# Optimization experiments

Measured on AMD Instinct MI355X. Metric: run time of the kernel, lower is better.

## Reference

```python
import jax, jax.numpy as jnp
import numpy as np

CONTEXT_LENGTH = 2048
D_MODEL = 1024
N_HEADS = 16
D_HEAD = 64
ROPE_BASE = 10000.0
STD = 0.02


def rope(x, sines, cosines):
    # x: [b, s, h, d]; sines/cosines: [s, d//2]; interleaved even/odd pairing
    x_even = x[..., ::2]
    x_odd = x[..., 1::2]
    c = cosines[None, :, None, :]
    s = sines[None, :, None, :]
    out_even = x_even * c - x_odd * s
    out_odd = x_even * s + x_odd * c
    return jnp.stack((out_even, out_odd), axis=-1).reshape(x.shape)


def setup_inputs() -> dict:
    key = jax.random.key(0)
    k1, k2, k3, k4, k5 = jax.random.split(key, 5)
    x = jax.random.normal(k1, (2, 2048, D_MODEL), dtype=jnp.float32)
    key_weight = STD * jax.random.normal(k2, (N_HEADS, D_HEAD, D_MODEL), dtype=jnp.float32)
    query_weight = STD * jax.random.normal(k3, (N_HEADS, D_HEAD, D_MODEL), dtype=jnp.float32)
    value_weight = STD * jax.random.normal(k4, (N_HEADS, D_HEAD, D_MODEL), dtype=jnp.float32)
    output_weight = STD * jax.random.normal(k5, (D_MODEL, N_HEADS, D_HEAD), dtype=jnp.float32)
    angles = ROPE_BASE ** (-2.0 * jnp.arange(D_HEAD // 2, dtype=jnp.float32) / D_HEAD)
    positions = jnp.arange(CONTEXT_LENGTH, dtype=jnp.float32)
    apos = positions[:, None] * angles[None, :]  # [context, d_head//2]
    sines = jnp.sin(apos)
    cosines = jnp.cos(apos)
    return {"x": x, "key_weight": key_weight, "query_weight": query_weight,
            "value_weight": value_weight, "output_weight": output_weight,
            "sines": sines, "cosines": cosines}


def reference(x, key_weight, query_weight, value_weight, output_weight, sines, cosines):
    s = x.shape[1]
    sn, cs = sines[:s], cosines[:s]
    keys = jnp.einsum('hdm,bpm->bphd', key_weight, x)
    queries = jnp.einsum('hdm,bpm->bphd', query_weight, x)
    values = jnp.einsum('hdm,bpm->bphd', value_weight, x)
    keys = rope(keys, sn, cs)
    queries = rope(queries, sn, cs)
    # NOTE: no 1/sqrt(d_head) scaling, faithful to source
    scores = jnp.einsum('bkhd,bqhd->bhqk', keys, queries)
    mask = jnp.tril(jnp.ones((s, s), dtype=bool))  # causal (task='next_token')
    scores = jnp.where(mask[None, None], scores, -jnp.inf)
    pattern = jax.nn.softmax(scores, axis=-1)
    outputs = jnp.einsum('bhqk,bkhd->bqhd', pattern, values)
    return jnp.einsum('mhd,bphd->bpm', output_weight, outputs)
```

## Files before the change

kernel.cpp:

```cpp
#include <hip/hip_runtime.h>
#include <hip/hip_bf16.h>
#include <stdint.h>

typedef __bf16 bf16_t;
typedef bf16_t bf16x8 __attribute__((ext_vector_type(8)));
typedef float  f32x4  __attribute__((ext_vector_type(4)));

#define GAS __attribute__((address_space(1)))
#define LAS __attribute__((address_space(3)))

__device__ inline void gld_lds16(const void* g, void* l) {
    __builtin_amdgcn_global_load_lds((const GAS void*)g, (LAS void*)l, 16, 0, 0);
}

__device__ inline int swz(int row, int colbyte) {
    return row * 128 + (colbyte ^ ((row & 7) << 4));
}

__global__ __launch_bounds__(256) void k_cvt5(const float* __restrict__ i0, bf16_t* __restrict__ o0,
                                              const float* __restrict__ i1, bf16_t* __restrict__ o1,
                                              const float* __restrict__ i2, bf16_t* __restrict__ o2,
                                              const float* __restrict__ i3, bf16_t* __restrict__ o3,
                                              const float* __restrict__ i4, bf16_t* __restrict__ o4) {
    const float* in; bf16_t* out; int n;
    switch (blockIdx.y) {
        case 0: in = i0; out = o0; n = 4194304; break;
        case 1: in = i1; out = o1; n = 1048576; break;
        case 2: in = i2; out = o2; n = 1048576; break;
        case 3: in = i3; out = o3; n = 1048576; break;
        default: in = i4; out = o4; n = 1048576; break;
    }
    int i = (blockIdx.x * 256 + threadIdx.x) * 8;
    if (i >= n) return;
    f32x4 v0 = *(const f32x4*)(in + i);
    f32x4 v1 = *(const f32x4*)(in + i + 4);
    bf16x8 o;
    o[0] = (bf16_t)v0[0]; o[1] = (bf16_t)v0[1]; o[2] = (bf16_t)v0[2]; o[3] = (bf16_t)v0[3];
    o[4] = (bf16_t)v1[0]; o[5] = (bf16_t)v1[1]; o[6] = (bf16_t)v1[2]; o[7] = (bf16_t)v1[3];
    *(bf16x8*)(out + i) = o;
}

__global__ __launch_bounds__(256) void k_rope(bf16_t* __restrict__ Q, bf16_t* __restrict__ Kt,
                                              const float* __restrict__ sn,
                                              const float* __restrict__ cs) {
    int idx = blockIdx.x * 256 + threadIdx.x;
    bf16_t* T = blockIdx.y ? Kt : Q;
    int row = idx >> 9;
    int pi  = idx & 511;
    int h = pi >> 5, i = pi & 31;
    int p = row & 2047;
    float c = cs[p * 32 + i], s = sn[p * 32 + i];
    bf16_t* ptr = T + (size_t)row * 1024 + h * 64 + 2 * i;
    float e = (float)ptr[0], o = (float)ptr[1];
    ptr[0] = (bf16_t)(e * c - o * s);
    ptr[1] = (bf16_t)(e * s + o * c);
}

template <typename OutT>
__global__ __launch_bounds__(256) void k_gemm_bt(
    const bf16_t* __restrict__ A,
    const bf16_t* __restrict__ B0, const bf16_t* __restrict__ B1,
    OutT* __restrict__ C0, OutT* __restrict__ C1,
    int M, int N, int K) {
    const bf16_t* B = blockIdx.z == 0 ? B0 : B1;
    OutT*         C = blockIdx.z == 0 ? C0 : C1;
    const int BK = 32;
    __shared__ bf16_t As[128 * BK];
    __shared__ bf16_t Bs[128 * BK];
    int tid = threadIdx.x;
    int lane = tid & 63, wid = tid >> 6;
    int row0 = blockIdx.y * 128, col0 = blockIdx.x * 128;
    int wr = (wid >> 1) * 64, wc = (wid & 1) * 64;
    int lr = lane & 15, kg = lane >> 4;

    f32x4 acc[4][4];
#pragma unroll
    for (int i = 0; i < 4; ++i)
#pragma unroll
        for (int j = 0; j < 4; ++j) acc[i][j] = (f32x4){0.f, 0.f, 0.f, 0.f};

    int ob = tid * 16;
    for (int k0 = 0; k0 < K; k0 += BK) {
        __syncthreads();
#pragma unroll
        for (int p = 0; p < 2; ++p) {
            int off = p * 4096 + ob;
            int r = off >> 6;
            int cb = off & 63;
            gld_lds16((const char*)A + ((size_t)(row0 + r) * K + k0) * 2 + cb, (char*)As + off);
            gld_lds16((const char*)B + ((size_t)(col0 + r) * K + k0) * 2 + cb, (char*)Bs + off);
        }
        __syncthreads();
        bf16x8 af[4], bfr[4];
#pragma unroll
        for (int mi = 0; mi < 4; ++mi)
            af[mi] = *(const bf16x8*)&As[(wr + mi * 16 + lr) * BK + kg * 8];
#pragma unroll
        for (int ni = 0; ni < 4; ++ni)
            bfr[ni] = *(const bf16x8*)&Bs[(wc + ni * 16 + lr) * BK + kg * 8];
#pragma unroll
        for (int mi = 0; mi < 4; ++mi)
#pragma unroll
            for (int ni = 0; ni < 4; ++ni)
                acc[mi][ni] = __builtin_amdgcn_mfma_f32_16x16x32_bf16(af[mi], bfr[ni],
                                                                      acc[mi][ni], 0, 0, 0);
    }
#pragma unroll
    for (int mi = 0; mi < 4; ++mi)
#pragma unroll
        for (int ni = 0; ni < 4; ++ni)
#pragma unroll
            for (int r = 0; r < 4; ++r) {
                int row = row0 + wr + mi * 16 + kg * 4 + r;
                int col = col0 + wc + ni * 16 + lr;
                C[(size_t)row * N + col] = (OutT)acc[mi][ni][r];
            }
}

__global__ __launch_bounds__(256) void k_flash(const bf16_t* __restrict__ Q,
                                               const bf16_t* __restrict__ Kt,
                                               const bf16_t* __restrict__ Vt,
                                               bf16_t* __restrict__ Ob) {
    const int DM = 1024, S = 2048;
    int qb = (blockIdx.y & 8) ? (31 - blockIdx.x) : blockIdx.x;
    int h = blockIdx.y, b = blockIdx.z;
    int tid = threadIdx.x, lane = tid & 63, wid = tid >> 6;
    int lr = lane & 15, kg = lane >> 4;
    int rowbase = b * S;
    int colbase = h * 64;

    __shared__ bf16_t Ks[2][64 * 64];
    __shared__ bf16_t Vs[2][64 * 64];
    __shared__ bf16_t Ps[4][16 * 64];

    int qrow0 = qb * 64 + wid * 16;
    bf16x8 qf[2];
#pragma unroll
    for (int s = 0; s < 2; ++s)
        qf[s] = *(const bf16x8*)&Q[(size_t)(rowbase + qrow0 + lr) * DM + colbase + s * 32 + kg * 8];

    f32x4 Oa[4];
    float m_run[4], l_run[4];
#pragma unroll
    for (int i = 0; i < 4; ++i) {
        Oa[i] = (f32x4){0.f, 0.f, 0.f, 0.f};
        m_run[i] = -1e30f;
        l_run[i] = 0.f;
    }

    int r0 = tid >> 3;
    int c0 = (tid & 7) * 8;
    const bf16_t* Kg = Kt + (size_t)rowbase * DM + colbase;
    const bf16_t* Vg = Vt + (size_t)colbase * 4096 + b * S;

    bf16x8 kr[2], vr[2];
#define LOADKV(kb, kr_, vr_)                                                      \
    _Pragma("unroll") for (int p = 0; p < 2; ++p) {                               \
        int r = p * 32 + r0;                                                      \
        kr_[p] = *(const bf16x8*)&Kg[(size_t)((kb) * 64 + r) * DM + c0];          \
        vr_[p] = *(const bf16x8*)&Vg[(size_t)r * 4096 + (kb) * 64 + c0];          \
    }
#define STOREKV(bi, kr_, vr_)                                                     \
    _Pragma("unroll") for (int p = 0; p < 2; ++p) {                               \
        int r = p * 32 + r0;                                                      \
        *(bf16x8*)((char*)&Ks[bi][0] + swz(r, c0 * 2)) = kr_[p];                  \
        *(bf16x8*)((char*)&Vs[bi][0] + swz(r, c0 * 2)) = vr_[p];                  \
    }

    LOADKV(0, kr, vr);
    STOREKV(0, kr, vr);
    __syncthreads();

    int cur = 0;
    for (int kb = 0; kb <= qb; ++kb) {
        bf16x8 kr2[2], vr2[2];
        if (kb < qb) { LOADKV(kb + 1, kr2, vr2); }

        f32x4 sa[4];
#pragma unroll
        for (int ni = 0; ni < 4; ++ni) sa[ni] = (f32x4){0.f, 0.f, 0.f, 0.f};
#pragma unroll
        for (int s = 0; s < 2; ++s)
#pragma unroll
            for (int ni = 0; ni < 4; ++ni) {
                bf16x8 kf = *(const bf16x8*)((char*)&Ks[cur][0] + swz(ni * 16 + lr, s * 64 + kg * 16));
                sa[ni] = __builtin_amdgcn_mfma_f32_16x16x32_bf16(qf[s], kf, sa[ni], 0, 0, 0);
            }

#pragma unroll
        for (int r = 0; r < 4; ++r) {
            int qpos = qrow0 + kg * 4 + r;
            float mx = -1e30f;
#pragma unroll
            for (int ni = 0; ni < 4; ++ni) {
                int ck = kb * 64 + ni * 16 + lr;
                float v = sa[ni][r];
                if (ck > qpos) { v = -1e30f; sa[ni][r] = v; }
                mx = fmaxf(mx, v);
            }
#pragma unroll
            for (int off = 1; off < 16; off <<= 1) mx = fmaxf(mx, __shfl_xor(mx, off));
            float mo = m_run[r];
            float mn = fmaxf(mo, mx);
            float scale = __expf(mo - mn);
            float rs = 0.f;
#pragma unroll
            for (int ni = 0; ni < 4; ++ni) {
                float pv = __expf(sa[ni][r] - mn);
                sa[ni][r] = pv;
                rs += pv;
            }
#pragma unroll
            for (int off = 1; off < 16; off <<= 1) rs += __shfl_xor(rs, off);
            l_run[r] = l_run[r] * scale + rs;
            m_run[r] = mn;
#pragma unroll
            for (int ni = 0; ni < 4; ++ni) Oa[ni][r] *= scale;
        }

#pragma unroll
        for (int r = 0; r < 4; ++r)
#pragma unroll
            for (int ni = 0; ni < 4; ++ni)
                *(bf16_t*)((char*)&Ps[wid][0] + swz(kg * 4 + r, (ni * 16 + lr) * 2)) =
                    (bf16_t)sa[ni][r];

#pragma unroll
        for (int s = 0; s < 2; ++s) {
            bf16x8 pf = *(const bf16x8*)((char*)&Ps[wid][0] + swz(lr, s * 64 + kg * 16));
#pragma unroll
            for (int ni = 0; ni < 4; ++ni) {
                bf16x8 vf = *(const bf16x8*)((char*)&Vs[cur][0] + swz(ni * 16 + lr, s * 64 + kg * 16));
                Oa[ni] = __builtin_amdgcn_mfma_f32_16x16x32_bf16(pf, vf, Oa[ni], 0, 0, 0);
            }
        }

        if (kb < qb) {
            STOREKV(cur ^ 1, kr2, vr2);
            __syncthreads();
            cur ^= 1;
        }
    }

#pragma unroll
    for (int r = 0; r < 4; ++r) {
        int row = rowbase + qrow0 + kg * 4 + r;
        float inv = 1.f / l_run[r];
#pragma unroll
        for (int ni = 0; ni < 4; ++ni)
            Ob[(size_t)row * DM + colbase + ni * 16 + lr] = (bf16_t)(Oa[ni][r] * inv);
    }
}

extern "C" void kernel_launch(void* const* d_in, const int* in_sizes, int n_in,
                              void* d_out, int out_size, void* d_ws, size_t ws_size,
                              hipStream_t stream) {
    const float* x  = (const float*)d_in[0];
    const float* wk = (const float*)d_in[1];
    const float* wq = (const float*)d_in[2];
    const float* wv = (const float*)d_in[3];
    const float* wo = (const float*)d_in[4];
    const float* sn = (const float*)d_in[5];
    const float* cs = (const float*)d_in[6];
    float* out = (float*)d_out;
    (void)in_sizes; (void)n_in; (void)out_size; (void)ws_size;

    char* ws = (char*)d_ws;
    const size_t MB = 1024 * 1024;
    bf16_t* xb  = (bf16_t*)(ws + 0);
    bf16_t* wqb = (bf16_t*)(ws + 8 * MB);
    bf16_t* wkb = (bf16_t*)(ws + 10 * MB);
    bf16_t* wvb = (bf16_t*)(ws + 12 * MB);
    bf16_t* wob = (bf16_t*)(ws + 14 * MB);
    bf16_t* Qb  = (bf16_t*)(ws + 16 * MB);
    bf16_t* Kb  = (bf16_t*)(ws + 24 * MB);
    bf16_t* Vtb = (bf16_t*)(ws + 32 * MB);
    bf16_t* Ob  = (bf16_t*)(ws + 40 * MB);

    k_cvt5<<<dim3(2048, 5), 256, 0, stream>>>(x, xb, wq, wqb, wk, wkb, wv, wvb, wo, wob);

    k_gemm_bt<bf16_t><<<dim3(8, 32, 2), 256, 0, stream>>>(
        xb, wqb, wkb, Qb, Kb, 4096, 1024, 1024);
    k_gemm_bt<bf16_t><<<dim3(32, 8, 1), 256, 0, stream>>>(
        wvb, xb, xb, Vtb, Vtb, 1024, 4096, 1024);

    k_rope<<<dim3(8192, 2), 256, 0, stream>>>(Qb, Kb, sn, cs);

    k_flash<<<dim3(32, 16, 2), 256, 0, stream>>>(Qb, Kb, Vtb, Ob);

    k_gemm_bt<float><<<dim3(8, 32, 1), 256, 0, stream>>>(
        Ob, wob, wob, out, out, 4096, 1024, 1024);
}
```

Measured before the change: 193.0 us.

## Make flash waves independent with register-held K/V and paired causal strips

The flash kernel changes so that each wave owns a 32-row query strip and handles two strips (j and 63-j) to balance the causal workload, with four independent waves per block. K and V fragments are now loaded straight from global memory into registers and double-buffered in registers, which removes shared-memory K/V staging and block-wide barriers. The causal mask is applied only on the diagonal tile. The cost is more register pressure and redundant global/L2 loads of K and V, since the four waves no longer share them through shared memory. The grid shrinks to 8x16x2 blocks.

```diff
diff --git a/kernel.cpp b/kernel.cpp
--- a/kernel.cpp
+++ b/kernel.cpp
@@ -118,138 +118,141 @@
 }
 
 __global__ __launch_bounds__(256) void k_flash(const bf16_t* __restrict__ Q,
-                                               const bf16_t* __restrict__ Kt,
+                                               const bf16_t* __restrict__ K,
                                                const bf16_t* __restrict__ Vt,
                                                bf16_t* __restrict__ Ob) {
-    const int DM = 1024, S = 2048;
-    int qb = (blockIdx.y & 8) ? (31 - blockIdx.x) : blockIdx.x;
+    const int DM = 1024, S = 2048, NB = 4096;
     int h = blockIdx.y, b = blockIdx.z;
     int tid = threadIdx.x, lane = tid & 63, wid = tid >> 6;
     int lr = lane & 15, kg = lane >> 4;
     int rowbase = b * S;
     int colbase = h * 64;
-
-    __shared__ bf16_t Ks[2][64 * 64];
-    __shared__ bf16_t Vs[2][64 * 64];
-    __shared__ bf16_t Ps[4][16 * 64];
-
-    int qrow0 = qb * 64 + wid * 16;
-    bf16x8 qf[2];
-#pragma unroll
-    for (int s = 0; s < 2; ++s)
-        qf[s] = *(const bf16x8*)&Q[(size_t)(rowbase + qrow0 + lr) * DM + colbase + s * 32 + kg * 8];
-
-    f32x4 Oa[4];
-    float m_run[4], l_run[4];
-#pragma unroll
-    for (int i = 0; i < 4; ++i) {
-        Oa[i] = (f32x4){0.f, 0.f, 0.f, 0.f};
-        m_run[i] = -1e30f;
-        l_run[i] = 0.f;
-    }
-
-    int r0 = tid >> 3;
-    int c0 = (tid & 7) * 8;
-    const bf16_t* Kg = Kt + (size_t)rowbase * DM + colbase;
-    const bf16_t* Vg = Vt + (size_t)colbase * 4096 + b * S;
-
-    bf16x8 kr[2], vr[2];
-#define LOADKV(kb, kr_, vr_)                                                      \
-    _Pragma("unroll") for (int p = 0; p < 2; ++p) {                               \
-        int r = p * 32 + r0;                                                      \
-        kr_[p] = *(const bf16x8*)&Kg[(size_t)((kb) * 64 + r) * DM + c0];          \
-        vr_[p] = *(const bf16x8*)&Vg[(size_t)r * 4096 + (kb) * 64 + c0];          \
-    }
-#define STOREKV(bi, kr_, vr_)                                                     \
-    _Pragma("unroll") for (int p = 0; p < 2; ++p) {                               \
-        int r = p * 32 + r0;                                                      \
-        *(bf16x8*)((char*)&Ks[bi][0] + swz(r, c0 * 2)) = kr_[p];                  \
-        *(bf16x8*)((char*)&Vs[bi][0] + swz(r, c0 * 2)) = vr_[p];                  \
-    }
-
-    LOADKV(0, kr, vr);
-    STOREKV(0, kr, vr);
-    __syncthreads();
-
-    int cur = 0;
-    for (int kb = 0; kb <= qb; ++kb) {
-        bf16x8 kr2[2], vr2[2];
-        if (kb < qb) { LOADKV(kb + 1, kr2, vr2); }
-
-        f32x4 sa[4];
-#pragma unroll
-        for (int ni = 0; ni < 4; ++ni) sa[ni] = (f32x4){0.f, 0.f, 0.f, 0.f};
-#pragma unroll
-        for (int s = 0; s < 2; ++s)
-#pragma unroll
-            for (int ni = 0; ni < 4; ++ni) {
-                bf16x8 kf = *(const bf16x8*)((char*)&Ks[cur][0] + swz(ni * 16 + lr, s * 64 + kg * 16));
-                sa[ni] = __builtin_amdgcn_mfma_f32_16x16x32_bf16(qf[s], kf, sa[ni], 0, 0, 0);
+    int j = blockIdx.x * 4 + wid;
+
+    __shared__ bf16_t Ps[4][32 * 64];
+    char* Pw = (char*)&Ps[wid][0];
+
+    const bf16_t* Kg = K + (size_t)rowbase * DM + colbase;
+    const bf16_t* Vg = Vt + (size_t)colbase * NB + rowbase;
+
+#define LOADK(kb, dst)                                                               \
+    _Pragma("unroll") for (int ni = 0; ni < 4; ++ni)                                 \
+    _Pragma("unroll") for (int s2 = 0; s2 < 2; ++s2)                                 \
+        dst[ni * 2 + s2] =                                                           \
+            *(const bf16x8*)&Kg[(size_t)((kb) * 64 + ni * 16 + lr) * DM + s2 * 32 + kg * 8];
+
+#define LOADV(kb, dst)                                                               \
+    _Pragma("unroll") for (int ni = 0; ni < 4; ++ni)                                 \
+    _Pragma("unroll") for (int s2 = 0; s2 < 2; ++s2)                                 \
+        dst[ni * 2 + s2] =                                                           \
+            *(const bf16x8*)&Vg[(size_t)(ni * 16 + lr) * NB + (kb) * 64 + s2 * 32 + kg * 8];
+
+#define STEP(kb, kf, vf, kfN, vfN)                                                   \
+    {                                                                                \
+        f32x4 sa[2][4];                                                              \
+        _Pragma("unroll") for (int mi = 0; mi < 2; ++mi)                             \
+        _Pragma("unroll") for (int ni = 0; ni < 4; ++ni)                             \
+            sa[mi][ni] = (f32x4){0.f, 0.f, 0.f, 0.f};                                \
+        _Pragma("unroll") for (int s2 = 0; s2 < 2; ++s2)                             \
+        _Pragma("unroll") for (int ni = 0; ni < 4; ++ni)                             \
+        _Pragma("unroll") for (int mi = 0; mi < 2; ++mi)                             \
+            sa[mi][ni] = __builtin_amdgcn_mfma_f32_16x16x32_bf16(                    \
+                qf[mi][s2], kf[ni * 2 + s2], sa[mi][ni], 0, 0, 0);                   \
+        if ((kb) < kbmax) { LOADK((kb) + 1, kfN); }                                  \
+        if ((kb) == kbmax) {                    \
+            _Pragma("unroll") for (int mi = 0; mi < 2; ++mi)                         \
+            _Pragma("unroll") for (int ni = 0; ni < 4; ++ni)                         \
+            _Pragma("unroll") for (int r = 0; r < 4; ++r)                            \
+                if ((kb) * 64 + ni * 16 + lr > spos + mi * 16 + kg * 4 + r)          \
+                    sa[mi][ni][r] = -1e30f;                                          \
+        }                                                                            \
+        _Pragma("unroll") for (int mi = 0; mi < 2; ++mi)                             \
+        _Pragma("unroll") for (int r = 0; r < 4; ++r) {                              \
+            float mx = fmaxf(fmaxf(sa[mi][0][r], sa[mi][1][r]),                      \
+                             fmaxf(sa[mi][2][r], sa[mi][3][r]));                     \
+            _Pragma("unroll") for (int off = 1; off < 16; off <<= 1)                 \
+                mx = fmaxf(mx, __shfl_xor(mx, off));                                 \
+            float mo = m_run[mi][r];                                                 \
+            float mn = fmaxf(mo, mx);                                                \
+            float sc = __expf(mo - mn);                                              \
+            float rs = 0.f;                                                          \
+            _Pragma("unroll") for (int ni = 0; ni < 4; ++ni) {                       \
+                float pv = __expf(sa[mi][ni][r] - mn);                               \
+                sa[mi][ni][r] = pv;                                                  \
+                rs += pv;                                                            \
+            }                                                                        \
+            _Pragma("unroll") for (int off = 1; off < 16; off <<= 1)                 \
+                rs += __shfl_xor(rs, off);                                           \
+            l_run[mi][r] = l_run[mi][r] * sc + rs;                                   \
+            m_run[mi][r] = mn;                                                       \
+            _Pragma("unroll") for (int ni = 0; ni < 4; ++ni) Oa[mi][ni][r] *= sc;    \
+        }                                                                            \
+        _Pragma("unroll") for (int mi = 0; mi < 2; ++mi)                             \
+        _Pragma("unroll") for (int r = 0; r < 4; ++r)                                \
+        _Pragma("unroll") for (int ni = 0; ni < 4; ++ni)                             \
+            *(bf16_t*)(Pw + swz(mi * 16 + kg * 4 + r, (ni * 16 + lr) * 2)) =         \
+                (bf16_t)sa[mi][ni][r];                                               \
+        _Pragma("unroll") for (int s2 = 0; s2 < 2; ++s2) {                           \
+            bf16x8 pf0 = *(const bf16x8*)(Pw + swz(lr, s2 * 64 + kg * 16));          \
+            bf16x8 pf1 = *(const bf16x8*)(Pw + swz(16 + lr, s2 * 64 + kg * 16));     \
+            _Pragma("unroll") for (int ni = 0; ni < 4; ++ni) {                       \
+                Oa[0][ni] = __builtin_amdgcn_mfma_f32_16x16x32_bf16(                 \
+                    pf0, vf[ni * 2 + s2], Oa[0][ni], 0, 0, 0);                       \
+                Oa[1][ni] = __builtin_amdgcn_mfma_f32_16x16x32_bf16(                 \
+                    pf1, vf[ni * 2 + s2], Oa[1][ni], 0, 0, 0);                       \
+            }                                                                        \
+        }                                                                            \
+        if ((kb) < kbmax) { LOADV((kb) + 1, vfN); }                                  \
+    }
+
+#pragma unroll 1
+    for (int half = 0; half < 2; ++half) {
+        int s = half ? (63 - j) : j;
+        int spos = s * 32;
+        int kbmax = s >> 1;
+
+        bf16x8 qf[2][2];
+#pragma unroll
+        for (int mi = 0; mi < 2; ++mi)
+#pragma unroll
+            for (int s2 = 0; s2 < 2; ++s2)
+                qf[mi][s2] = *(const bf16x8*)&Q[(size_t)(rowbase + spos + mi * 16 + lr) * DM +
+                                                colbase + s2 * 32 + kg * 8];
+
+        f32x4 Oa[2][4];
+        float m_run[2][4], l_run[2][4];
+#pragma unroll
+        for (int mi = 0; mi < 2; ++mi)
+#pragma unroll
+            for (int ni = 0; ni < 4; ++ni) Oa[mi][ni] = (f32x4){0.f, 0.f, 0.f, 0.f};
+#pragma unroll
+        for (int mi = 0; mi < 2; ++mi)
+#pragma unroll
+            for (int r = 0; r < 4; ++r) { m_run[mi][r] = -1e30f; l_run[mi][r] = 0.f; }
+
+        bf16x8 kfA[8], kfB[8], vfA[8], vfB[8];
+        LOADK(0, kfA);
+        LOADV(0, vfA);
+#pragma unroll 1
+        for (int kb = 0; kb <= kbmax; kb += 2) {
+            STEP(kb, kfA, vfA, kfB, vfB);
+            if (kb + 1 <= kbmax) STEP(kb + 1, kfB, vfB, kfA, vfA);
+        }
+
+#pragma unroll
+        for (int mi = 0; mi < 2; ++mi)
+#pragma unroll
+            for (int r = 0; r < 4; ++r) {
+                float inv = 1.f / l_run[mi][r];
+                size_t row = (size_t)(rowbase + spos + mi * 16 + kg * 4 + r);
+#pragma unroll
+                for (int ni = 0; ni < 4; ++ni)
+                    Ob[row * DM + colbase + ni * 16 + lr] = (bf16_t)(Oa[mi][ni][r] * inv);
             }
-
-#pragma unroll
-        for (int r = 0; r < 4; ++r) {
-            int qpos = qrow0 + kg * 4 + r;
-            float mx = -1e30f;
-#pragma unroll
-            for (int ni = 0; ni < 4; ++ni) {
-                int ck = kb * 64 + ni * 16 + lr;
-                float v = sa[ni][r];
-                if (ck > qpos) { v = -1e30f; sa[ni][r] = v; }
-                mx = fmaxf(mx, v);
-            }
-#pragma unroll
-            for (int off = 1; off < 16; off <<= 1) mx = fmaxf(mx, __shfl_xor(mx, off));
-            float mo = m_run[r];
-            float mn = fmaxf(mo, mx);
-            float scale = __expf(mo - mn);
-            float rs = 0.f;
-#pragma unroll
-            for (int ni = 0; ni < 4; ++ni) {
-                float pv = __expf(sa[ni][r] - mn);
-                sa[ni][r] = pv;
-                rs += pv;
-            }
-#pragma unroll
-            for (int off = 1; off < 16; off <<= 1) rs += __shfl_xor(rs, off);
-            l_run[r] = l_run[r] * scale + rs;
-            m_run[r] = mn;
-#pragma unroll
-            for (int ni = 0; ni < 4; ++ni) Oa[ni][r] *= scale;
-        }
-
-#pragma unroll
-        for (int r = 0; r < 4; ++r)
-#pragma unroll
-            for (int ni = 0; ni < 4; ++ni)
-                *(bf16_t*)((char*)&Ps[wid][0] + swz(kg * 4 + r, (ni * 16 + lr) * 2)) =
-                    (bf16_t)sa[ni][r];
-
-#pragma unroll
-        for (int s = 0; s < 2; ++s) {
-            bf16x8 pf = *(const bf16x8*)((char*)&Ps[wid][0] + swz(lr, s * 64 + kg * 16));
-#pragma unroll
-            for (int ni = 0; ni < 4; ++ni) {
-                bf16x8 vf = *(const bf16x8*)((char*)&Vs[cur][0] + swz(ni * 16 + lr, s * 64 + kg * 16));
-                Oa[ni] = __builtin_amdgcn_mfma_f32_16x16x32_bf16(pf, vf, Oa[ni], 0, 0, 0);
-            }
-        }
-
-        if (kb < qb) {
-            STOREKV(cur ^ 1, kr2, vr2);
-            __syncthreads();
-            cur ^= 1;
-        }
-    }
-
-#pragma unroll
-    for (int r = 0; r < 4; ++r) {
-        int row = rowbase + qrow0 + kg * 4 + r;
-        float inv = 1.f / l_run[r];
-#pragma unroll
-        for (int ni = 0; ni < 4; ++ni)
-            Ob[(size_t)row * DM + colbase + ni * 16 + lr] = (bf16_t)(Oa[ni][r] * inv);
-    }
+    }
+#undef LOADK
+#undef LOADV
+#undef STEP
 }
 
 extern "C" void kernel_launch(void* const* d_in, const int* in_sizes, int n_in,
@@ -286,7 +289,7 @@
 
     k_rope<<<dim3(8192, 2), 256, 0, stream>>>(Qb, Kb, sn, cs);
 
-    k_flash<<<dim3(32, 16, 2), 256, 0, stream>>>(Qb, Kb, Vtb, Ob);
+    k_flash<<<dim3(8, 16, 2), 256, 0, stream>>>(Qb, Kb, Vtb, Ob);
 
     k_gemm_bt<float><<<dim3(8, 32, 1), 256, 0, stream>>>(
         Ob, wob, wob, out, out, 4096, 1024, 1024);
```

New measurement: 192.1 us. No clear change (-0.4%).
